# Performance work log

Measured on AMD Instinct MI355X. Metric: run time of the kernel, lower is better.

Reference implementation:

```python
import jax, jax.numpy as jnp
import numpy as np

N_NODES = 100000
N_EDGES = 1600000
IN_CH = 128
EDGE_CH = 32
HEADS = 4
OUT_CH = 32
NEG_SLOPE = 0.2
EPS = 1e-16  # matches torch_geometric softmax denominator epsilon


def setup_inputs() -> dict:
    key = jax.random.key(0)
    ks = jax.random.split(key, 8)
    x = jax.random.normal(ks[0], (N_NODES, IN_CH), dtype=jnp.float32)
    edge_attr = jax.random.normal(ks[1], (N_EDGES, EDGE_CH), dtype=jnp.float32)
    # glorot-ish scaled params
    Wl = jax.random.normal(ks[2], (HEADS * OUT_CH, IN_CH), dtype=jnp.float32) * (1.0 / np.sqrt(IN_CH))
    We = jax.random.normal(ks[3], (HEADS * OUT_CH, EDGE_CH), dtype=jnp.float32) * (1.0 / np.sqrt(EDGE_CH))
    att_l = jax.random.normal(ks[4], (1, HEADS, OUT_CH), dtype=jnp.float32) * 0.1
    att_r = jax.random.normal(ks[5], (1, HEADS, OUT_CH), dtype=jnp.float32) * 0.1
    att_e = jax.random.normal(ks[6], (1, HEADS, OUT_CH), dtype=jnp.float32) * 0.1
    bias = jnp.zeros((HEADS * OUT_CH,), dtype=jnp.float32)
    edge_index = jax.random.randint(ks[7], (2, N_EDGES), 0, N_NODES, dtype=jnp.int32)
    return {"x": x, "edge_attr": edge_attr, "Wl": Wl, "We": We,
            "att_l": att_l, "att_r": att_r, "att_e": att_e,
            "bias": bias, "edge_index": edge_index}


def reference(x, edge_attr, Wl, We, att_l, att_r, att_e, bias, edge_index):
    N = x.shape[0]
    H, C = att_l.shape[1], att_l.shape[2]
    # shared lin_l == lin_r projection  [N, H, C]
    xl = (x @ Wl.T).reshape(N, H, C)
    alpha_l = (xl * att_l).sum(-1)          # [N, H] source term
    alpha_r = (xl * att_r).sum(-1)          # [N, H] target term
    # edge feature projection            [E, H, C]
    e = (edge_attr @ We.T).reshape(-1, H, C)
    alpha_e = (e * att_e).sum(-1)           # [E, H]
    src, dst = edge_index[0], edge_index[1]
    # per-edge attention logits
    alpha = alpha_l[src] + alpha_r[dst] + alpha_e        # [E, H]
    alpha = jax.nn.leaky_relu(alpha, NEG_SLOPE)
    # segment softmax over incoming edges of each target node
    amax = jax.ops.segment_max(alpha, dst, num_segments=N)   # [N, H]
    ex = jnp.exp(alpha - amax[dst])
    denom = jax.ops.segment_sum(ex, dst, num_segments=N)     # [N, H]
    alpha_n = ex / (denom[dst] + EPS)                        # [E, H]
    # weighted scatter-add aggregation of source features
    msg = xl[src] * alpha_n[:, :, None]                      # [E, H, C]
    out = jax.ops.segment_sum(msg, dst, num_segments=N)      # [N, H, C]
    out = out.reshape(N, H * C) + bias                       # concat heads
    return out
```

## Files before the change

kernel.cpp:

```cpp
#include <hip/hip_runtime.h>

#define NN 100000
#define NE 1600000
#define NB 391
#define NEG 0.2f

#define OFF_XLB   ((size_t)0)
#define OFF_AL    ((size_t)6400000)
#define OFF_AR    ((size_t)6800000)
#define OFF_WE    ((size_t)7200000)
#define OFF_ALPHA ((size_t)7200128)
#define OFF_SRC   ((size_t)13600128)
#define OFF_TMP   OFF_SRC
#define OFF_BSUM  (OFF_SRC + 110000)
#define OFF_DEG   ((size_t)15200128)
#define OFF_ROW   ((size_t)15300128)

__device__ __forceinline__ unsigned short f2bf(float f) {
    unsigned u = __float_as_uint(f);
    u += 0x7fffu + ((u >> 16) & 1u);
    return (unsigned short)(u >> 16);
}
__device__ __forceinline__ float bf2f(unsigned short v) {
    return __uint_as_float((unsigned)v << 16);
}

__global__ void k_prep_zero(const float* __restrict__ We, const float* __restrict__ att_e,
                            float* __restrict__ we, int* __restrict__ deg) {
    int i = blockIdx.x * 256 + threadIdx.x;
    if (i < NN) deg[i] = 0;
    if (blockIdx.x == 0 && threadIdx.x < 128) {
        int t = threadIdx.x, h = t >> 5, k = t & 31;
        float s = 0.f;
        for (int c = 0; c < 32; ++c)
            s += att_e[h * 32 + c] * We[(size_t)(h * 32 + c) * 32 + k];
        we[t] = s;
    }
}

__global__ void k_hist(const int* __restrict__ ei, int* __restrict__ deg) {
    int e = blockIdx.x * 256 + threadIdx.x;
    atomicAdd(&deg[ei[NE + e]], 1);
}

__global__ __launch_bounds__(256, 2) void k_node(
        const float* __restrict__ x, const float* __restrict__ Wl,
        const float* __restrict__ attl, const float* __restrict__ attr_,
        unsigned short* __restrict__ xlb, float* __restrict__ al, float* __restrict__ ar) {
    __shared__ float wT[128 * 128];
    __shared__ float xT[128 * 32];
    int t = threadIdx.x;
    int og = t & 31, ng = t >> 5;
    int nb = blockIdx.x * 32;

    {
        int o = t & 127, q = t >> 7;
        #pragma unroll
        for (int chunk = 0; chunk < 16; ++chunk) {
            int k0 = chunk * 8 + q * 4;
            float4 w = *(const float4*)&Wl[(size_t)o * 128 + k0];
            wT[(k0 + 0) * 128 + o] = w.x;
            wT[(k0 + 1) * 128 + o] = w.y;
            wT[(k0 + 2) * 128 + o] = w.z;
            wT[(k0 + 3) * 128 + o] = w.w;
        }
    }
    {
        int n = t & 31, q = t >> 5;
        #pragma unroll
        for (int chunk = 0; chunk < 4; ++chunk) {
            int k0 = chunk * 32 + q * 4;
            float4 v = *(const float4*)&x[(size_t)(nb + n) * 128 + k0];
            xT[(k0 + 0) * 32 + n] = v.x;
            xT[(k0 + 1) * 32 + n] = v.y;
            xT[(k0 + 2) * 32 + n] = v.z;
            xT[(k0 + 3) * 32 + n] = v.w;
        }
    }
    float4 attl4 = *(const float4*)&attl[og * 4];
    float4 attr4 = *(const float4*)&attr_[og * 4];
    __syncthreads();

    float4 a0 = make_float4(0,0,0,0), a1 = a0, a2 = a0, a3 = a0;
    #pragma unroll 8
    for (int k = 0; k < 128; ++k) {
        float4 w  = *(const float4*)&wT[k * 128 + og * 4];
        float4 xv = *(const float4*)&xT[k * 32  + ng * 4];
        a0.x += w.x * xv.x; a0.y += w.y * xv.x; a0.z += w.z * xv.x; a0.w += w.w * xv.x;
        a1.x += w.x * xv.y; a1.y += w.y * xv.y; a1.z += w.z * xv.y; a1.w += w.w * xv.y;
        a2.x += w.x * xv.z; a2.y += w.y * xv.z; a2.z += w.z * xv.z; a2.w += w.w * xv.z;
        a3.x += w.x * xv.w; a3.y += w.y * xv.w; a3.z += w.z * xv.w; a3.w += w.w * xv.w;
    }

    float4 accs[4] = {a0, a1, a2, a3};
    #pragma unroll
    for (int j = 0; j < 4; ++j) {
        int node = nb + ng * 4 + j;
        ushort4 pk;
        pk.x = f2bf(accs[j].x); pk.y = f2bf(accs[j].y);
        pk.z = f2bf(accs[j].z); pk.w = f2bf(accs[j].w);
        *(ushort4*)&xlb[(size_t)node * 128 + og * 4] = pk;
        float pl = accs[j].x * attl4.x + accs[j].y * attl4.y +
                   accs[j].z * attl4.z + accs[j].w * attl4.w;
        float pr = accs[j].x * attr4.x + accs[j].y * attr4.y +
                   accs[j].z * attr4.z + accs[j].w * attr4.w;
        #pragma unroll
        for (int off = 1; off <= 4; off <<= 1) {
            pl += __shfl_xor(pl, off);
            pr += __shfl_xor(pr, off);
        }
        if ((og & 7) == 0) {
            al[(size_t)node * 4 + (og >> 3)] = pl;
            ar[(size_t)node * 4 + (og >> 3)] = pr;
        }
    }
}

__global__ void k_scan_block(const int* __restrict__ deg, int* __restrict__ row_tmp,
                             int* __restrict__ bsum) {
    __shared__ int sh[256];
    int t = threadIdx.x, i = blockIdx.x * 256 + t;
    int d = (i < NN) ? deg[i] : 0;
    int v = d;
    sh[t] = v; __syncthreads();
    for (int off = 1; off < 256; off <<= 1) {
        int add = (t >= off) ? sh[t - off] : 0;
        __syncthreads();
        v += add; sh[t] = v; __syncthreads();
    }
    if (i < NN) row_tmp[i] = v - d;
    if (t == 255) bsum[blockIdx.x] = v;
}

__global__ void k_scan_top(int* __restrict__ bsum) {
    __shared__ int sh[512];
    int t = threadIdx.x;
    int d = (t < NB) ? bsum[t] : 0;
    int v = d;
    sh[t] = v; __syncthreads();
    for (int off = 1; off < 512; off <<= 1) {
        int add = (t >= off) ? sh[t - off] : 0;
        __syncthreads();
        v += add; sh[t] = v; __syncthreads();
    }
    if (t < NB) bsum[t] = v - d;
}

__global__ void k_scan_add(const int* __restrict__ row_tmp, const int* __restrict__ bsum,
                           int* __restrict__ row, int* __restrict__ cursor) {
    int i = blockIdx.x * 256 + threadIdx.x;
    if (i < NN) {
        int v = row_tmp[i] + bsum[i >> 8];
        row[i] = v;
        cursor[i] = v;
    }
    if (i == 0) row[NN] = NE;
}

__global__ __launch_bounds__(256) void k_scatter(
        const float* __restrict__ eattr, const int* __restrict__ ei,
        const float* __restrict__ al, const float* __restrict__ ar,
        const float* __restrict__ we, int* __restrict__ cursor,
        int* __restrict__ csr_src, float* __restrict__ alpha_s) {
    __shared__ __align__(16) float wsh[128];
    if (threadIdx.x < 128) wsh[threadIdx.x] = we[threadIdx.x];
    __syncthreads();
    int e = blockIdx.x * 256 + threadIdx.x;
    int src = ei[e], dst = ei[NE + e];
    const float4* ea = (const float4*)(eattr + (size_t)e * 32);
    float a[4] = {0.f, 0.f, 0.f, 0.f};
    #pragma unroll
    for (int r = 0; r < 8; ++r) {
        float4 v = ea[r];
        #pragma unroll
        for (int h = 0; h < 4; ++h) {
            float4 w = *(const float4*)&wsh[h * 32 + r * 4];
            a[h] += v.x * w.x + v.y * w.y + v.z * w.z + v.w * w.w;
        }
    }
    float4 ls = *(const float4*)&al[(size_t)src * 4];
    float4 rs = *(const float4*)&ar[(size_t)dst * 4];
    a[0] += ls.x + rs.x; a[1] += ls.y + rs.y;
    a[2] += ls.z + rs.z; a[3] += ls.w + rs.w;
    #pragma unroll
    for (int h = 0; h < 4; ++h) a[h] = a[h] > 0.f ? a[h] : NEG * a[h];
    int slot = atomicAdd(&cursor[dst], 1);
    csr_src[slot] = src;
    *(float4*)&alpha_s[(size_t)slot * 4] = make_float4(a[0], a[1], a[2], a[3]);
}

__global__ __launch_bounds__(128) void k_out(
        const int* __restrict__ row, const int* __restrict__ csr_src,
        const float* __restrict__ alpha_s, const unsigned short* __restrict__ xlb,
        const float* __restrict__ bias, float* __restrict__ out) {
    int n = blockIdx.x;
    int t = threadIdx.x, h = t >> 5;
    int s0 = row[n], s1 = row[n + 1];

    float m0 = -1e30f, m1 = -1e30f, m2 = -1e30f, m3 = -1e30f;
    int s = s0;
    for (; s + 4 <= s1; s += 4) {
        m0 = fmaxf(m0, alpha_s[(size_t)(s + 0) * 4 + h]);
        m1 = fmaxf(m1, alpha_s[(size_t)(s + 1) * 4 + h]);
        m2 = fmaxf(m2, alpha_s[(size_t)(s + 2) * 4 + h]);
        m3 = fmaxf(m3, alpha_s[(size_t)(s + 3) * 4 + h]);
    }
    for (; s < s1; ++s) m0 = fmaxf(m0, alpha_s[(size_t)s * 4 + h]);
    float m = fmaxf(fmaxf(m0, m1), fmaxf(m2, m3));

    float l0 = 0.f, l1 = 0.f, l2 = 0.f, l3 = 0.f;
    float O0 = 0.f, O1 = 0.f, O2 = 0.f, O3 = 0.f;
    s = s0;
    for (; s + 4 <= s1; s += 4) {
        int src0 = csr_src[s + 0], src1 = csr_src[s + 1];
        int src2 = csr_src[s + 2], src3 = csr_src[s + 3];
        float a0 = alpha_s[(size_t)(s + 0) * 4 + h];
        float a1 = alpha_s[(size_t)(s + 1) * 4 + h];
        float a2 = alpha_s[(size_t)(s + 2) * 4 + h];
        float a3 = alpha_s[(size_t)(s + 3) * 4 + h];
        unsigned short v0 = xlb[(size_t)src0 * 128 + t];
        unsigned short v1 = xlb[(size_t)src1 * 128 + t];
        unsigned short v2 = xlb[(size_t)src2 * 128 + t];
        unsigned short v3 = xlb[(size_t)src3 * 128 + t];
        float e0 = __expf(a0 - m), e1 = __expf(a1 - m);
        float e2 = __expf(a2 - m), e3 = __expf(a3 - m);
        l0 += e0; l1 += e1; l2 += e2; l3 += e3;
        O0 += e0 * bf2f(v0); O1 += e1 * bf2f(v1);
        O2 += e2 * bf2f(v2); O3 += e3 * bf2f(v3);
    }
    for (; s < s1; ++s) {
        float a = alpha_s[(size_t)s * 4 + h];
        unsigned short v = xlb[(size_t)csr_src[s] * 128 + t];
        float e = __expf(a - m);
        l0 += e; O0 += e * bf2f(v);
    }
    float l = (l0 + l1) + (l2 + l3);
    float O = (O0 + O1) + (O2 + O3);
    out[(size_t)n * 128 + t] = O / (l + 1e-16f) + bias[t];
}

extern "C" void kernel_launch(void* const* d_in, const int* in_sizes, int n_in,
                              void* d_out, int out_size, void* d_ws, size_t ws_size,
                              hipStream_t stream) {
    const float* x     = (const float*)d_in[0];
    const float* eattr = (const float*)d_in[1];
    const float* Wl    = (const float*)d_in[2];
    const float* We    = (const float*)d_in[3];
    const float* att_l = (const float*)d_in[4];
    const float* att_r = (const float*)d_in[5];
    const float* att_e = (const float*)d_in[6];
    const float* bias  = (const float*)d_in[7];
    const int*   ei    = (const int*)d_in[8];
    float* out = (float*)d_out;

    float* ws = (float*)d_ws;
    unsigned short* xlb = (unsigned short*)(ws + OFF_XLB);
    float* al      = ws + OFF_AL;
    float* ar      = ws + OFF_AR;
    float* we      = ws + OFF_WE;
    float* alpha_s = ws + OFF_ALPHA;
    int*   csr_src = (int*)(ws + OFF_SRC);
    int*   row_tmp = (int*)(ws + OFF_TMP);
    int*   bsum    = (int*)(ws + OFF_BSUM);
    int*   deg     = (int*)(ws + OFF_DEG);
    int*   rowp    = (int*)(ws + OFF_ROW);

    k_prep_zero<<<NB, 256, 0, stream>>>(We, att_e, we, deg);
    k_hist<<<NE / 256, 256, 0, stream>>>(ei, deg);
    k_node<<<NN / 32, 256, 0, stream>>>(x, Wl, att_l, att_r, xlb, al, ar);
    k_scan_block<<<NB, 256, 0, stream>>>(deg, row_tmp, bsum);
    k_scan_top<<<1, 512, 0, stream>>>(bsum);
    k_scan_add<<<NB, 256, 0, stream>>>(row_tmp, bsum, rowp, deg);
    k_scatter<<<NE / 256, 256, 0, stream>>>(eattr, ei, al, ar, we, deg, csr_src, alpha_s);
    k_out<<<NN, 128, 0, stream>>>(rowp, csr_src, alpha_s, xlb, bias, out);
}
```

Before: 680.0 us.

## Write edge logits coalesced, store edge ids in CSR, use online softmax

The edge kernel now writes attention logits in edge order, which is coalesced, and stores only the edge id at the atomically claimed CSR slot, where before it scattered both the source index and a float4 to random slots. The output kernel replaces its separate max pass with a single-pass online softmax that rescales the running sums. The cost is an extra level of indirection in the aggregation: each edge needs an eidx load, then a dependent load of the source from edge_index, then a random gather of the logits. Those gathers were sequential before.

```diff
diff --git a/kernel.cpp b/kernel.cpp
--- a/kernel.cpp
+++ b/kernel.cpp
@@ -10,9 +10,9 @@
 #define OFF_AR    ((size_t)6800000)
 #define OFF_WE    ((size_t)7200000)
 #define OFF_ALPHA ((size_t)7200128)
-#define OFF_SRC   ((size_t)13600128)
-#define OFF_TMP   OFF_SRC
-#define OFF_BSUM  (OFF_SRC + 110000)
+#define OFF_EIDX  ((size_t)13600128)
+#define OFF_TMP   OFF_EIDX
+#define OFF_BSUM  (OFF_EIDX + 110000)
 #define OFF_DEG   ((size_t)15200128)
 #define OFF_ROW   ((size_t)15300128)
 
@@ -157,11 +157,11 @@
     if (i == 0) row[NN] = NE;
 }
 
-__global__ __launch_bounds__(256) void k_scatter(
+__global__ __launch_bounds__(256) void k_edge(
         const float* __restrict__ eattr, const int* __restrict__ ei,
         const float* __restrict__ al, const float* __restrict__ ar,
         const float* __restrict__ we, int* __restrict__ cursor,
-        int* __restrict__ csr_src, float* __restrict__ alpha_s) {
+        int* __restrict__ eidx, float* __restrict__ alpha_e) {
     __shared__ __align__(16) float wsh[128];
     if (threadIdx.x < 128) wsh[threadIdx.x] = we[threadIdx.x];
     __syncthreads();
@@ -184,55 +184,60 @@
     a[2] += ls.z + rs.z; a[3] += ls.w + rs.w;
     #pragma unroll
     for (int h = 0; h < 4; ++h) a[h] = a[h] > 0.f ? a[h] : NEG * a[h];
+    *(float4*)&alpha_e[(size_t)e * 4] = make_float4(a[0], a[1], a[2], a[3]);
     int slot = atomicAdd(&cursor[dst], 1);
-    csr_src[slot] = src;
-    *(float4*)&alpha_s[(size_t)slot * 4] = make_float4(a[0], a[1], a[2], a[3]);
+    eidx[slot] = e;
 }
 
 __global__ __launch_bounds__(128) void k_out(
-        const int* __restrict__ row, const int* __restrict__ csr_src,
-        const float* __restrict__ alpha_s, const unsigned short* __restrict__ xlb,
+        const int* __restrict__ row, const int* __restrict__ eidx,
+        const int* __restrict__ ei, const float* __restrict__ alpha_e,
+        const unsigned short* __restrict__ xlb,
         const float* __restrict__ bias, float* __restrict__ out) {
     int n = blockIdx.x;
     int t = threadIdx.x, h = t >> 5;
     int s0 = row[n], s1 = row[n + 1];
 
-    float m0 = -1e30f, m1 = -1e30f, m2 = -1e30f, m3 = -1e30f;
+    float m = -1e30f;
+    float l0 = 0.f, l1 = 0.f, l2 = 0.f, l3 = 0.f;
+    float O0 = 0.f, O1 = 0.f, O2 = 0.f, O3 = 0.f;
     int s = s0;
     for (; s + 4 <= s1; s += 4) {
-        m0 = fmaxf(m0, alpha_s[(size_t)(s + 0) * 4 + h]);
-        m1 = fmaxf(m1, alpha_s[(size_t)(s + 1) * 4 + h]);
-        m2 = fmaxf(m2, alpha_s[(size_t)(s + 2) * 4 + h]);
-        m3 = fmaxf(m3, alpha_s[(size_t)(s + 3) * 4 + h]);
-    }
-    for (; s < s1; ++s) m0 = fmaxf(m0, alpha_s[(size_t)s * 4 + h]);
-    float m = fmaxf(fmaxf(m0, m1), fmaxf(m2, m3));
-
-    float l0 = 0.f, l1 = 0.f, l2 = 0.f, l3 = 0.f;
-    float O0 = 0.f, O1 = 0.f, O2 = 0.f, O3 = 0.f;
-    s = s0;
-    for (; s + 4 <= s1; s += 4) {
-        int src0 = csr_src[s + 0], src1 = csr_src[s + 1];
-        int src2 = csr_src[s + 2], src3 = csr_src[s + 3];
-        float a0 = alpha_s[(size_t)(s + 0) * 4 + h];
-        float a1 = alpha_s[(size_t)(s + 1) * 4 + h];
-        float a2 = alpha_s[(size_t)(s + 2) * 4 + h];
-        float a3 = alpha_s[(size_t)(s + 3) * 4 + h];
+        int e0 = eidx[s + 0], e1 = eidx[s + 1];
+        int e2 = eidx[s + 2], e3 = eidx[s + 3];
+        int src0 = ei[e0], src1 = ei[e1], src2 = ei[e2], src3 = ei[e3];
+        float a0 = alpha_e[(size_t)e0 * 4 + h];
+        float a1 = alpha_e[(size_t)e1 * 4 + h];
+        float a2 = alpha_e[(size_t)e2 * 4 + h];
+        float a3 = alpha_e[(size_t)e3 * 4 + h];
         unsigned short v0 = xlb[(size_t)src0 * 128 + t];
         unsigned short v1 = xlb[(size_t)src1 * 128 + t];
         unsigned short v2 = xlb[(size_t)src2 * 128 + t];
         unsigned short v3 = xlb[(size_t)src3 * 128 + t];
-        float e0 = __expf(a0 - m), e1 = __expf(a1 - m);
-        float e2 = __expf(a2 - m), e3 = __expf(a3 - m);
-        l0 += e0; l1 += e1; l2 += e2; l3 += e3;
-        O0 += e0 * bf2f(v0); O1 += e1 * bf2f(v1);
-        O2 += e2 * bf2f(v2); O3 += e3 * bf2f(v3);
+        float gm = fmaxf(fmaxf(a0, a1), fmaxf(a2, a3));
+        float nm = fmaxf(m, gm);
+        float sc = __expf(m - nm);
+        l0 *= sc; l1 *= sc; l2 *= sc; l3 *= sc;
+        O0 *= sc; O1 *= sc; O2 *= sc; O3 *= sc;
+        m = nm;
+        float x0 = __expf(a0 - m), x1 = __expf(a1 - m);
+        float x2 = __expf(a2 - m), x3 = __expf(a3 - m);
+        l0 += x0; l1 += x1; l2 += x2; l3 += x3;
+        O0 += x0 * bf2f(v0); O1 += x1 * bf2f(v1);
+        O2 += x2 * bf2f(v2); O3 += x3 * bf2f(v3);
     }
     for (; s < s1; ++s) {
-        float a = alpha_s[(size_t)s * 4 + h];
-        unsigned short v = xlb[(size_t)csr_src[s] * 128 + t];
-        float e = __expf(a - m);
-        l0 += e; O0 += e * bf2f(v);
+        int e = eidx[s];
+        int srcn = ei[e];
+        float a = alpha_e[(size_t)e * 4 + h];
+        float nm = fmaxf(m, a);
+        float sc = __expf(m - nm);
+        l0 *= sc; l1 *= sc; l2 *= sc; l3 *= sc;
+        O0 *= sc; O1 *= sc; O2 *= sc; O3 *= sc;
+        m = nm;
+        float x = __expf(a - m);
+        l0 += x;
+        O0 += x * bf2f(xlb[(size_t)srcn * 128 + t]);
     }
     float l = (l0 + l1) + (l2 + l3);
     float O = (O0 + O1) + (O2 + O3);
@@ -258,8 +263,8 @@
     float* al      = ws + OFF_AL;
     float* ar      = ws + OFF_AR;
     float* we      = ws + OFF_WE;
-    float* alpha_s = ws + OFF_ALPHA;
-    int*   csr_src = (int*)(ws + OFF_SRC);
+    float* alpha_e = ws + OFF_ALPHA;
+    int*   eidx    = (int*)(ws + OFF_EIDX);
     int*   row_tmp = (int*)(ws + OFF_TMP);
     int*   bsum    = (int*)(ws + OFF_BSUM);
     int*   deg     = (int*)(ws + OFF_DEG);
@@ -271,6 +276,6 @@
     k_scan_block<<<NB, 256, 0, stream>>>(deg, row_tmp, bsum);
     k_scan_top<<<1, 512, 0, stream>>>(bsum);
     k_scan_add<<<NB, 256, 0, stream>>>(row_tmp, bsum, rowp, deg);
-    k_scatter<<<NE / 256, 256, 0, stream>>>(eattr, ei, al, ar, we, deg, csr_src, alpha_s);
-    k_out<<<NN, 128, 0, stream>>>(rowp, csr_src, alpha_s, xlb, bias, out);
-}
+    k_edge<<<NE / 256, 256, 0, stream>>>(eattr, ei, al, ar, we, deg, eidx, alpha_e);
+    k_out<<<NN, 128, 0, stream>>>(rowp, eidx, ei, alpha_e, xlb, bias, out);
+}
```

After: 727.6 us. 1.07x slower.

## Precompute exp in edge kernel, pack src+fp16 weights into 16B record, drop max pass

Applied to the files above, without the earlier changes.

The edge kernel now applies exp (with the logit clamped at 60) and stores the four per-head weights as fp16 together with the source index in one 16-byte record. The output kernel no longer makes a separate segment-max pass. It reads one vector record per edge instead of separate csr_src and alpha loads. The cost is that softmax stability now relies on the clamp and the fp16 range, with reduced precision in the weights.

```diff
diff --git a/kernel.cpp b/kernel.cpp
--- a/kernel.cpp
+++ b/kernel.cpp
@@ -1,4 +1,5 @@
 #include <hip/hip_runtime.h>
+#include <hip/hip_fp16.h>
 
 #define NN 100000
 #define NE 1600000
@@ -9,10 +10,9 @@
 #define OFF_AL    ((size_t)6400000)
 #define OFF_AR    ((size_t)6800000)
 #define OFF_WE    ((size_t)7200000)
-#define OFF_ALPHA ((size_t)7200128)
-#define OFF_SRC   ((size_t)13600128)
-#define OFF_TMP   OFF_SRC
-#define OFF_BSUM  (OFF_SRC + 110000)
+#define OFF_REC   ((size_t)7200128)
+#define OFF_TMP   ((size_t)13600128)
+#define OFF_BSUM  (OFF_TMP + 110000)
 #define OFF_DEG   ((size_t)15200128)
 #define OFF_ROW   ((size_t)15300128)
 
@@ -157,11 +157,11 @@
     if (i == 0) row[NN] = NE;
 }
 
-__global__ __launch_bounds__(256) void k_scatter(
+__global__ __launch_bounds__(256) void k_edge(
         const float* __restrict__ eattr, const int* __restrict__ ei,
         const float* __restrict__ al, const float* __restrict__ ar,
         const float* __restrict__ we, int* __restrict__ cursor,
-        int* __restrict__ csr_src, float* __restrict__ alpha_s) {
+        float4* __restrict__ rec) {
     __shared__ __align__(16) float wsh[128];
     if (threadIdx.x < 128) wsh[threadIdx.x] = we[threadIdx.x];
     __syncthreads();
@@ -183,56 +183,63 @@
     a[0] += ls.x + rs.x; a[1] += ls.y + rs.y;
     a[2] += ls.z + rs.z; a[3] += ls.w + rs.w;
     #pragma unroll
-    for (int h = 0; h < 4; ++h) a[h] = a[h] > 0.f ? a[h] : NEG * a[h];
+    for (int h = 0; h < 4; ++h) {
+        float v = a[h] > 0.f ? a[h] : NEG * a[h];
+        a[h] = __expf(fminf(v, 60.f));
+    }
+    __half2 h01 = __floats2half2_rn(a[0], a[1]);
+    __half2 h23 = __floats2half2_rn(a[2], a[3]);
     int slot = atomicAdd(&cursor[dst], 1);
-    csr_src[slot] = src;
-    *(float4*)&alpha_s[(size_t)slot * 4] = make_float4(a[0], a[1], a[2], a[3]);
+    float4 r;
+    r.x = __uint_as_float((unsigned)src);
+    r.y = *reinterpret_cast<float*>(&h01);
+    r.z = *reinterpret_cast<float*>(&h23);
+    r.w = 0.f;
+    rec[slot] = r;
+}
+
+__device__ __forceinline__ float pick_p(const float4& r, int h) {
+    __half2 h01 = *reinterpret_cast<const __half2*>(&r.y);
+    __half2 h23 = *reinterpret_cast<const __half2*>(&r.z);
+    float2 p01 = __half22float2(h01);
+    float2 p23 = __half22float2(h23);
+    float lo = (h & 2) ? p23.x : p01.x;
+    float hi = (h & 2) ? p23.y : p01.y;
+    return (h & 1) ? hi : lo;
 }
 
 __global__ __launch_bounds__(128) void k_out(
-        const int* __restrict__ row, const int* __restrict__ csr_src,
-        const float* __restrict__ alpha_s, const unsigned short* __restrict__ xlb,
+        const int* __restrict__ row, const float4* __restrict__ rec,
+        const unsigned short* __restrict__ xlb,
         const float* __restrict__ bias, float* __restrict__ out) {
     int n = blockIdx.x;
     int t = threadIdx.x, h = t >> 5;
     int s0 = row[n], s1 = row[n + 1];
 
-    float m0 = -1e30f, m1 = -1e30f, m2 = -1e30f, m3 = -1e30f;
+    float l0 = 0.f, l1 = 0.f, l2 = 0.f, l3 = 0.f;
+    float O0 = 0.f, O1 = 0.f, O2 = 0.f, O3 = 0.f;
     int s = s0;
     for (; s + 4 <= s1; s += 4) {
-        m0 = fmaxf(m0, alpha_s[(size_t)(s + 0) * 4 + h]);
-        m1 = fmaxf(m1, alpha_s[(size_t)(s + 1) * 4 + h]);
-        m2 = fmaxf(m2, alpha_s[(size_t)(s + 2) * 4 + h]);
-        m3 = fmaxf(m3, alpha_s[(size_t)(s + 3) * 4 + h]);
-    }
-    for (; s < s1; ++s) m0 = fmaxf(m0, alpha_s[(size_t)s * 4 + h]);
-    float m = fmaxf(fmaxf(m0, m1), fmaxf(m2, m3));
-
-    float l0 = 0.f, l1 = 0.f, l2 = 0.f, l3 = 0.f;
-    float O0 = 0.f, O1 = 0.f, O2 = 0.f, O3 = 0.f;
-    s = s0;
-    for (; s + 4 <= s1; s += 4) {
-        int src0 = csr_src[s + 0], src1 = csr_src[s + 1];
-        int src2 = csr_src[s + 2], src3 = csr_src[s + 3];
-        float a0 = alpha_s[(size_t)(s + 0) * 4 + h];
-        float a1 = alpha_s[(size_t)(s + 1) * 4 + h];
-        float a2 = alpha_s[(size_t)(s + 2) * 4 + h];
-        float a3 = alpha_s[(size_t)(s + 3) * 4 + h];
+        float4 r0 = rec[s + 0], r1 = rec[s + 1];
+        float4 r2 = rec[s + 2], r3 = rec[s + 3];
+        int src0 = (int)__float_as_uint(r0.x), src1 = (int)__float_as_uint(r1.x);
+        int src2 = (int)__float_as_uint(r2.x), src3 = (int)__float_as_uint(r3.x);
         unsigned short v0 = xlb[(size_t)src0 * 128 + t];
         unsigned short v1 = xlb[(size_t)src1 * 128 + t];
         unsigned short v2 = xlb[(size_t)src2 * 128 + t];
         unsigned short v3 = xlb[(size_t)src3 * 128 + t];
-        float e0 = __expf(a0 - m), e1 = __expf(a1 - m);
-        float e2 = __expf(a2 - m), e3 = __expf(a3 - m);
-        l0 += e0; l1 += e1; l2 += e2; l3 += e3;
-        O0 += e0 * bf2f(v0); O1 += e1 * bf2f(v1);
-        O2 += e2 * bf2f(v2); O3 += e3 * bf2f(v3);
+        float p0 = pick_p(r0, h), p1 = pick_p(r1, h);
+        float p2 = pick_p(r2, h), p3 = pick_p(r3, h);
+        l0 += p0; l1 += p1; l2 += p2; l3 += p3;
+        O0 += p0 * bf2f(v0); O1 += p1 * bf2f(v1);
+        O2 += p2 * bf2f(v2); O3 += p3 * bf2f(v3);
     }
     for (; s < s1; ++s) {
-        float a = alpha_s[(size_t)s * 4 + h];
-        unsigned short v = xlb[(size_t)csr_src[s] * 128 + t];
-        float e = __expf(a - m);
-        l0 += e; O0 += e * bf2f(v);
+        float4 r = rec[s];
+        int srcn = (int)__float_as_uint(r.x);
+        float p = pick_p(r, h);
+        l0 += p;
+        O0 += p * bf2f(xlb[(size_t)srcn * 128 + t]);
     }
     float l = (l0 + l1) + (l2 + l3);
     float O = (O0 + O1) + (O2 + O3);
@@ -258,8 +265,7 @@
     float* al      = ws + OFF_AL;
     float* ar      = ws + OFF_AR;
     float* we      = ws + OFF_WE;
-    float* alpha_s = ws + OFF_ALPHA;
-    int*   csr_src = (int*)(ws + OFF_SRC);
+    float4* rec    = (float4*)(ws + OFF_REC);
     int*   row_tmp = (int*)(ws + OFF_TMP);
     int*   bsum    = (int*)(ws + OFF_BSUM);
     int*   deg     = (int*)(ws + OFF_DEG);
@@ -271,6 +277,6 @@
     k_scan_block<<<NB, 256, 0, stream>>>(deg, row_tmp, bsum);
     k_scan_top<<<1, 512, 0, stream>>>(bsum);
     k_scan_add<<<NB, 256, 0, stream>>>(row_tmp, bsum, rowp, deg);
-    k_scatter<<<NE / 256, 256, 0, stream>>>(eattr, ei, al, ar, we, deg, csr_src, alpha_s);
-    k_out<<<NN, 128, 0, stream>>>(rowp, csr_src, alpha_s, xlb, bias, out);
-}
+    k_edge<<<NE / 256, 256, 0, stream>>>(eattr, ei, al, ar, we, deg, rec);
+    k_out<<<NN, 128, 0, stream>>>(rowp, rec, xlb, bias, out);
+}
```

Result: faster. 651.3 us (-4.2%).
